# Performance work log

Measured on AMD Instinct MI355X. Metric: run time of the kernel, lower is better.

## Reference

```python
import jax, jax.numpy as jnp
import numpy as np

VOCAB, EMB, HID, LAT = 32000, 512, 1024, 512
B, T = 32, 128


def setup_inputs() -> dict:
    key = jax.random.key(0)
    ks = jax.random.split(key, 10)
    s = 0.02
    return {
        "latent_vector": jax.random.normal(ks[0], (B, LAT), jnp.float32),
        "target_tokens": jax.random.randint(ks[1], (B, T), 0, VOCAB),
        "emb": jax.random.normal(ks[2], (VOCAB, EMB), jnp.float32) * s,
        "W_lh": jax.random.normal(ks[3], (HID, LAT), jnp.float32) * s,
        "b_lh": jnp.zeros((HID,), jnp.float32),
        "W_ih": jax.random.normal(ks[4], (4 * HID, EMB), jnp.float32) * s,
        "b_ih": jnp.zeros((4 * HID,), jnp.float32),
        "W_hh": jax.random.normal(ks[5], (4 * HID, HID), jnp.float32) * s,
        "b_hh": jnp.zeros((4 * HID,), jnp.float32),
        "W_out": jax.random.normal(ks[6], (VOCAB, HID), jnp.float32) * s,
        "b_out": jnp.zeros((VOCAB,), jnp.float32),
    }


def reference(latent_vector, target_tokens, emb, W_lh, b_lh, W_ih, b_ih, W_hh, b_hh, W_out, b_out):
    # teacher_forcing_ratio = 1.0 (deterministic): input at step t is target_tokens[:, t-1]
    h = latent_vector @ W_lh.T + b_lh            # [B, HID]
    c = jnp.zeros_like(h)
    xs = emb[target_tokens[:, :-1]]              # [B, T-1, EMB]
    xs = jnp.swapaxes(xs, 0, 1)                  # [T-1, B, EMB]

    def step(carry, x):
        h, c = carry
        gates = x @ W_ih.T + b_ih + h @ W_hh.T + b_hh   # [B, 4*HID]
        i, f, g, o = jnp.split(gates, 4, axis=-1)       # PyTorch LSTM gate order
        c = jax.nn.sigmoid(f) * c + jax.nn.sigmoid(i) * jnp.tanh(g)
        h = jax.nn.sigmoid(o) * jnp.tanh(c)
        logits = h @ W_out.T + b_out                    # [B, VOCAB]
        return (h, c), logits

    _, logits = jax.lax.scan(step, (h, c), xs)          # [T-1, B, VOCAB]
    return jnp.swapaxes(logits, 0, 1)                   # [B, T-1, VOCAB]
```

## Files before the change

kernel.cpp:

```cpp
#include <hip/hip_runtime.h>
#include <cstdint>

typedef __bf16 bf16x8 __attribute__((ext_vector_type(8)));
typedef __bf16 bf16x4 __attribute__((ext_vector_type(4)));
typedef float  f32x4  __attribute__((ext_vector_type(4)));

#define VOCAB 32000
#define EMB   512
#define HID   1024
#define LAT   512
#define BATCH 32
#define TSTEP 127
#define MROWS 4064
#define MPAD  4096
#define G4    4096
#define NBLK  128
#define FSTRIDE 64

__device__ __forceinline__ float sigf(float x){ return 1.0f / (1.0f + __expf(-x)); }
__device__ __forceinline__ float tanhfast(float x){
    float ax = fabsf(x);
    float e  = __expf(-2.0f * ax);
    float t  = (1.0f - e) / (1.0f + e);
    return copysignf(t, x);
}

__device__ __forceinline__ void gll16(void* lds, const void* gsrc){
    __builtin_amdgcn_global_load_lds(
        (const __attribute__((address_space(1))) unsigned int*)gsrc,
        (__attribute__((address_space(3))) unsigned int*)lds,
        16, 0, 0);
}

__global__ __launch_bounds__(256) void cvt_kernel(
    const float* __restrict__ in, __bf16* __restrict__ out, int n4)
{
    int i = blockIdx.x * 256 + threadIdx.x;
    if (i < n4){
        float4 v = ((const float4*)in)[i];
        bf16x4 o = { (__bf16)v.x, (__bf16)v.y, (__bf16)v.z, (__bf16)v.w };
        ((bf16x4*)out)[i] = o;
    }
}

__global__ __launch_bounds__(256) void init_kernel(
    const float* __restrict__ latent,
    const float* __restrict__ Wlh,
    const float* __restrict__ blh,
    __bf16* __restrict__ h0,
    __bf16* __restrict__ Hall,
    unsigned* __restrict__ flags)
{
    if (blockIdx.x == 0 && threadIdx.x < NBLK)
        flags[threadIdx.x * FSTRIDE] = 0u;

    int id = blockIdx.x * 256 + threadIdx.x;
    int b = id >> 10, j = id & 1023;
    float s = blh[j];
    const float4* lr = (const float4*)(latent + (size_t)b * LAT);
    const float4* wr = (const float4*)(Wlh + (size_t)j * LAT);
    for (int k = 0; k < LAT / 4; ++k){
        float4 a = lr[k], w = wr[k];
        s += a.x * w.x + a.y * w.y + a.z * w.z + a.w * w.w;
    }
    h0[id] = (__bf16)s;
    Hall[(size_t)MROWS * HID + id] = (__bf16)0.0f;
}

__global__ __launch_bounds__(256) void gemm_xg(
    const float* __restrict__ emb,
    const float* __restrict__ Wih,
    const int*   __restrict__ tok,
    float*       __restrict__ xg,
    const float* __restrict__ bih,
    const float* __restrict__ bhh)
{
    __shared__ __bf16 As[2][128 * 32];
    __shared__ __bf16 Bs[2][128 * 32];

    const int tid  = threadIdx.x;
    const int wid  = tid >> 6, lane = tid & 63;
    const int tile_n = blockIdx.x, tile_m = blockIdx.y;
    const int wr = wid >> 1, wc = wid & 1;

    f32x4 acc[4][4] = {};

    auto stage = [&](int kt, int buf){
        #pragma unroll
        for (int j = 0; j < 2; ++j){
            const int slot = tid + j * 256;
            const int row  = slot >> 2;
            const int kb   = kt * 32 + (slot & 3) * 8;
            {
                const int brow = tile_n * 128 + row;
                const float4* p = (const float4*)(Wih + (size_t)brow * EMB + kb);
                float4 u = p[0], v = p[1];
                bf16x8 w = { (__bf16)u.x, (__bf16)u.y, (__bf16)u.z, (__bf16)u.w,
                             (__bf16)v.x, (__bf16)v.y, (__bf16)v.z, (__bf16)v.w };
                *(bf16x8*)&Bs[buf][row * 32 + (slot & 3) * 8] = w;
            }
            {
                int r = tile_m * 128 + row;
                int rc = (r < MROWS) ? r : (MROWS - 1);
                int token = tok[(rc & 31) * 128 + (rc >> 5)];
                const float4* p = (const float4*)(emb + (size_t)token * EMB + kb);
                float4 u = p[0], v = p[1];
                bf16x8 w = { (__bf16)u.x, (__bf16)u.y, (__bf16)u.z, (__bf16)u.w,
                             (__bf16)v.x, (__bf16)v.y, (__bf16)v.z, (__bf16)v.w };
                *(bf16x8*)&As[buf][row * 32 + (slot & 3) * 8] = w;
            }
        }
    };

    const int KT = EMB / 32;
    stage(0, 0);
    for (int kt = 0; kt < KT; ++kt){
        const int buf = kt & 1;
        __syncthreads();
        if (kt + 1 < KT) stage(kt + 1, buf ^ 1);
        const __bf16* Abuf = As[buf];
        const __bf16* Bbuf = Bs[buf];
        const int ar = lane & 15, ko = (lane >> 4) * 8;
        bf16x8 av[4], bv[4];
        #pragma unroll
        for (int m = 0; m < 4; ++m)
            av[m] = *(const bf16x8*)&Abuf[(wr * 64 + m * 16 + ar) * 32 + ko];
        #pragma unroll
        for (int n = 0; n < 4; ++n)
            bv[n] = *(const bf16x8*)&Bbuf[(wc * 64 + n * 16 + ar) * 32 + ko];
        #pragma unroll
        for (int m = 0; m < 4; ++m)
            #pragma unroll
            for (int n = 0; n < 4; ++n)
                acc[m][n] = __builtin_amdgcn_mfma_f32_16x16x32_bf16(av[m], bv[n], acc[m][n], 0, 0, 0);
    }

    const int r0 = tile_m * 128 + wr * 64 + ((lane >> 4) << 2);
    const int c0 = tile_n * 128 + wc * 64 + (lane & 15);
    #pragma unroll
    for (int m = 0; m < 4; ++m){
        #pragma unroll
        for (int n = 0; n < 4; ++n){
            const int col = c0 + n * 16;
            float badd = bih[col] + bhh[col];
            #pragma unroll
            for (int q = 0; q < 4; ++q){
                int row = r0 + m * 16 + q;
                xg[(size_t)row * G4 + col] = acc[m][n][q] + badd;
            }
        }
    }
}

template<int BF16B>
__global__ __launch_bounds__(256) void gemm_logits(
    const __bf16* __restrict__ A,
    const float*  __restrict__ Bf,
    const __bf16* __restrict__ Bb,
    float*        __restrict__ C,
    const float*  __restrict__ bias)
{
    __shared__ __bf16 As[2][128 * 32];
    __shared__ __bf16 Bs[2][128 * 32];

    const int tid  = threadIdx.x;
    const int wid  = tid >> 6, lane = tid & 63;
    const int tile_n = blockIdx.x, tile_m = blockIdx.y;
    const int wr = wid >> 1, wc = wid & 1;

    f32x4 acc[4][4] = {};

    auto stage = [&](int kt, int buf){
        const int kb = kt * 32 + (lane & 3) * 8;
        #pragma unroll
        for (int c2 = 0; c2 < 2; ++c2){
            int rA = tile_m * 128 + c2 * 64 + wid * 16 + (lane >> 2);
            gll16(&As[buf][c2 * 2048 + wid * 512], A + (size_t)rA * HID + kb);
            if constexpr (BF16B){
                int rB = tile_n * 128 + c2 * 64 + wid * 16 + (lane >> 2);
                gll16(&Bs[buf][c2 * 2048 + wid * 512], Bb + (size_t)rB * HID + kb);
            }
        }
        if constexpr (!BF16B){
            #pragma unroll
            for (int j = 0; j < 2; ++j){
                const int slot = tid + j * 256;
                const int row  = slot >> 2;
                const int kb2  = kt * 32 + (slot & 3) * 8;
                const int brow = tile_n * 128 + row;
                const float4* p = (const float4*)(Bf + (size_t)brow * HID + kb2);
                float4 u = p[0], v = p[1];
                bf16x8 w = { (__bf16)u.x, (__bf16)u.y, (__bf16)u.z, (__bf16)u.w,
                             (__bf16)v.x, (__bf16)v.y, (__bf16)v.z, (__bf16)v.w };
                *(bf16x8*)&Bs[buf][row * 32 + (slot & 3) * 8] = w;
            }
        }
    };

    const int KT = HID / 32;
    stage(0, 0);
    for (int kt = 0; kt < KT; ++kt){
        const int buf = kt & 1;
        __syncthreads();
        if (kt + 1 < KT) stage(kt + 1, buf ^ 1);
        const __bf16* Abuf = As[buf];
        const __bf16* Bbuf = Bs[buf];
        const int ar = lane & 15, ko = (lane >> 4) * 8;
        bf16x8 av[4], bv[4];
        #pragma unroll
        for (int m = 0; m < 4; ++m)
            av[m] = *(const bf16x8*)&Abuf[(wr * 64 + m * 16 + ar) * 32 + ko];
        #pragma unroll
        for (int n = 0; n < 4; ++n)
            bv[n] = *(const bf16x8*)&Bbuf[(wc * 64 + n * 16 + ar) * 32 + ko];
        #pragma unroll
        for (int m = 0; m < 4; ++m)
            #pragma unroll
            for (int n = 0; n < 4; ++n)
                acc[m][n] = __builtin_amdgcn_mfma_f32_16x16x32_bf16(av[m], bv[n], acc[m][n], 0, 0, 0);
    }

    const int r0 = tile_m * 128 + wr * 64 + ((lane >> 4) << 2);
    const int c0 = tile_n * 128 + wc * 64 + (lane & 15);
    #pragma unroll
    for (int m = 0; m < 4; ++m){
        #pragma unroll
        for (int n = 0; n < 4; ++n){
            const int col = c0 + n * 16;
            float badd = bias[col];
            #pragma unroll
            for (int q = 0; q < 4; ++q){
                int row = r0 + m * 16 + q;
                if (row < MROWS){
                    int t = row >> 5, b = row & 31;
                    __builtin_nontemporal_store(acc[m][n][q] + badd,
                        &C[((size_t)b * TSTEP + t) * VOCAB + col]);
                }
            }
        }
    }
}

__global__ __launch_bounds__(256) void lstm_coop(
    const float*  __restrict__ xg,
    __bf16*       __restrict__ Hall,
    __bf16*       __restrict__ hbuf,
    const __bf16* __restrict__ Whhb,
    unsigned*     __restrict__ flags)
{
    __shared__ float lds_g[4 * 4 * 4 * 64];
    const int tid = threadIdx.x, wid = tid >> 6, lane = tid & 63;
    const int jb = blockIdx.x * 8;

    bf16x8 bfrag[2][8];
    {
        const int gl = lane & 15, ko = (lane >> 4) * 8;
        #pragma unroll
        for (int nt = 0; nt < 2; ++nt){
            int gg = nt * 16 + gl;
            const __bf16* base =
                Whhb + (size_t)((gg >> 3) * HID + jb + (gg & 7)) * HID + wid * 256 + ko;
            #pragma unroll
            for (int ks = 0; ks < 8; ++ks)
                bfrag[nt][ks] = *(const bf16x8*)(base + ks * 32);
        }
    }

    const int b2 = tid >> 2, up0 = (tid & 3) * 2;
    const int mt2 = b2 >> 4, r2 = b2 & 15, reg2 = r2 & 3, lb2 = (r2 >> 2) << 4;
    float cst[2] = {0.0f, 0.0f};

    const float* xq = xg + (size_t)b2 * G4 + jb + up0;
    float2 xv[4];
    if (tid < 128){
        #pragma unroll
        for (int g = 0; g < 4; ++g) xv[g] = *(const float2*)(xq + g * HID);
    }

    const size_t e0 = (size_t)(lane & 15) * HID + wid * 256 + (lane >> 4) * 8;

    for (int t = 0; t < TSTEP; ++t){
        unsigned long long* hq = (unsigned long long*)(hbuf + (size_t)(t & 1) * (BATCH * HID));
        union { unsigned long long q[2]; bf16x8 v; } xa[16];
        #pragma unroll
        for (int ks = 0; ks < 8; ++ks){
            size_t q0 = (e0 + (size_t)ks * 32) >> 2;
            size_t q1 = q0 + ((size_t)16 * HID >> 2);
            xa[ks].q[0]     = __hip_atomic_load(hq + q0,     __ATOMIC_RELAXED, __HIP_MEMORY_SCOPE_AGENT);
            xa[ks].q[1]     = __hip_atomic_load(hq + q0 + 1, __ATOMIC_RELAXED, __HIP_MEMORY_SCOPE_AGENT);
            xa[8 + ks].q[0] = __hip_atomic_load(hq + q1,     __ATOMIC_RELAXED, __HIP_MEMORY_SCOPE_AGENT);
            xa[8 + ks].q[1] = __hip_atomic_load(hq + q1 + 1, __ATOMIC_RELAXED, __HIP_MEMORY_SCOPE_AGENT);
        }
        f32x4 a00 = {}, a01 = {}, a10 = {}, a11 = {};
        #pragma unroll
        for (int ks = 0; ks < 8; ++ks){
            a00 = __builtin_amdgcn_mfma_f32_16x16x32_bf16(xa[ks].v,     bfrag[0][ks], a00, 0, 0, 0);
            a01 = __builtin_amdgcn_mfma_f32_16x16x32_bf16(xa[ks].v,     bfrag[1][ks], a01, 0, 0, 0);
            a10 = __builtin_amdgcn_mfma_f32_16x16x32_bf16(xa[8 + ks].v, bfrag[0][ks], a10, 0, 0, 0);
            a11 = __builtin_amdgcn_mfma_f32_16x16x32_bf16(xa[8 + ks].v, bfrag[1][ks], a11, 0, 0, 0);
        }
        #pragma unroll
        for (int q = 0; q < 4; ++q){
            lds_g[((0 * 4 + wid) * 4 + q) * 64 + lane] = a00[q];
            lds_g[((1 * 4 + wid) * 4 + q) * 64 + lane] = a01[q];
            lds_g[((2 * 4 + wid) * 4 + q) * 64 + lane] = a10[q];
            lds_g[((3 * 4 + wid) * 4 + q) * 64 + lane] = a11[q];
        }
        __syncthreads();

        if (tid < 128){
            const float* xn = xq + (size_t)(t + 1) * (BATCH * G4);
            float2 xnew[4];
            #pragma unroll
            for (int g = 0; g < 4; ++g) xnew[g] = *(const float2*)(xn + g * HID);

            float h2[2];
            #pragma unroll
            for (int du = 0; du < 2; ++du){
                int u2 = up0 + du;
                float gate[4];
                #pragma unroll
                for (int ty = 0; ty < 4; ++ty){
                    int gg = ty * 8 + u2;
                    int mtnt = mt2 * 2 + (gg >> 4);
                    int li = lb2 | (gg & 15);
                    float s = 0.0f;
                    #pragma unroll
                    for (int w = 0; w < 4; ++w)
                        s += lds_g[((mtnt * 4 + w) * 4 + reg2) * 64 + li];
                    gate[ty] = s;
                }
                float gi = gate[0] + ((du == 0) ? xv[0].x : xv[0].y);
                float gf = gate[1] + ((du == 0) ? xv[1].x : xv[1].y);
                float gc = gate[2] + ((du == 0) ? xv[2].x : xv[2].y);
                float go = gate[3] + ((du == 0) ? xv[3].x : xv[3].y);
                float c = sigf(gf) * cst[du] + sigf(gi) * tanhfast(gc);
                cst[du] = c;
                h2[du] = sigf(go) * tanhfast(c);
            }
            #pragma unroll
            for (int g = 0; g < 4; ++g) xv[g] = xnew[g];

            union { __bf16 h[2]; unsigned u; } pk;
            pk.h[0] = (__bf16)h2[0]; pk.h[1] = (__bf16)h2[1];
            unsigned* hw = (unsigned*)(hbuf + (size_t)((t + 1) & 1) * (BATCH * HID)
                                       + (size_t)b2 * HID + jb + up0);
            __hip_atomic_store(hw, pk.u, __ATOMIC_RELAXED, __HIP_MEMORY_SCOPE_AGENT);
            *(unsigned*)(Hall + ((size_t)t * BATCH + b2) * HID + jb + up0) = pk.u;
        }

        if (t + 1 == TSTEP) break;

        __syncthreads();
        if (wid == 0){
            if (lane == 0){
                __hip_atomic_store(&flags[blockIdx.x * FSTRIDE], (unsigned)(t + 1),
                                   __ATOMIC_RELAXED, __HIP_MEMORY_SCOPE_AGENT);
            }
            const unsigned tgt = (unsigned)(t + 1);
            for (;;){
                unsigned f0 = __hip_atomic_load(&flags[lane * FSTRIDE],
                                  __ATOMIC_RELAXED, __HIP_MEMORY_SCOPE_AGENT);
                unsigned f1 = __hip_atomic_load(&flags[(lane + 64) * FSTRIDE],
                                  __ATOMIC_RELAXED, __HIP_MEMORY_SCOPE_AGENT);
                if (f0 >= tgt && f1 >= tgt) break;
                __builtin_amdgcn_s_sleep(1);
            }
        }
        __syncthreads();
    }
}

extern "C" void kernel_launch(void* const* d_in, const int* in_sizes, int n_in,
                              void* d_out, int out_size, void* d_ws, size_t ws_size,
                              hipStream_t stream)
{
    const float* latent = (const float*)d_in[0];
    const int*   tokens = (const int*)d_in[1];
    const float* emb    = (const float*)d_in[2];
    const float* Wlh    = (const float*)d_in[3];
    const float* blh    = (const float*)d_in[4];
    const float* Wih    = (const float*)d_in[5];
    const float* bih    = (const float*)d_in[6];
    const float* Whh    = (const float*)d_in[7];
    const float* bhh    = (const float*)d_in[8];
    const float* Wout   = (const float*)d_in[9];
    const float* bout   = (const float*)d_in[10];
    float* out = (float*)d_out;

    const size_t xg_b   = (size_t)MPAD * G4 * 4;
    const size_t hall_b = (size_t)MPAD * HID * 2;
    const size_t whh_b  = (size_t)G4 * HID * 2;
    const size_t wout_b = (size_t)VOCAB * HID * 2;
    const size_t hb_b   = (size_t)2 * BATCH * HID * 2;
    const size_t cnt_b  = (size_t)NBLK * FSTRIDE * 4;

    char* p = (char*)d_ws;
    const bool wsA = ws_size >= xg_b + hall_b + whh_b + wout_b + hb_b + cnt_b;
    const bool wsB = ws_size >= hall_b + whh_b + wout_b + hb_b + cnt_b;

    float* xg;
    if (wsA){ xg = (float*)p; p += xg_b; }
    else    { xg = (float*)d_out; }
    __bf16* Hall = (__bf16*)p; p += hall_b;
    __bf16* Whhb = (__bf16*)p; p += whh_b;
    __bf16* Woutb = nullptr;
    if (wsA || wsB){ Woutb = (__bf16*)p; p += wout_b; }
    __bf16* hbuf = (__bf16*)p; p += hb_b;
    unsigned* flags = (unsigned*)p; p += cnt_b;

    cvt_kernel<<<dim3(G4 * HID / 4 / 256), dim3(256), 0, stream>>>(
        Whh, Whhb, G4 * HID / 4);

    init_kernel<<<dim3(128), dim3(256), 0, stream>>>(latent, Wlh, blh, hbuf, Hall, flags);

    gemm_xg<<<dim3(G4 / 128, MPAD / 128), dim3(256), 0, stream>>>(
        emb, Wih, tokens, xg, bih, bhh);

    if (Woutb)
        cvt_kernel<<<dim3(VOCAB * HID / 4 / 256), dim3(256), 0, stream>>>(
            Wout, Woutb, VOCAB * HID / 4);

    {
        const float*  xgc   = xg;
        __bf16*       hallp = Hall;
        __bf16*       hbp   = hbuf;
        const __bf16* whhp  = Whhb;
        unsigned*     flagp = flags;
        void* args[] = { (void*)&xgc, (void*)&hallp, (void*)&hbp, (void*)&whhp, (void*)&flagp };
        hipLaunchCooperativeKernel((void*)lstm_coop, dim3(NBLK), dim3(256), args, 0, stream);
    }

    if (Woutb)
        gemm_logits<1><<<dim3(VOCAB / 128, MPAD / 128), dim3(256), 0, stream>>>(
            Hall, (const float*)nullptr, Woutb, out, bout);
    else
        gemm_logits<0><<<dim3(VOCAB / 128, MPAD / 128), dim3(256), 0, stream>>>(
            Hall, Wout, (const __bf16*)nullptr, out, bout);
}
```

Baseline: 1.313 ms.

## Overlap W_out bf16 conversion with LSTM and swizzle logits GEMM tile order

```diff
diff --git a/kernel.cpp b/kernel.cpp
--- a/kernel.cpp
+++ b/kernel.cpp
@@ -152,6 +152,8 @@
     }
 }
 
+#define NTM 32
+#define NTN 250
 template<int BF16B>
 __global__ __launch_bounds__(256) void gemm_logits(
     const __bf16* __restrict__ A,
@@ -165,7 +167,13 @@
 
     const int tid  = threadIdx.x;
     const int wid  = tid >> 6, lane = tid & 63;
-    const int tile_n = blockIdx.x, tile_m = blockIdx.y;
+
+    const int bid = blockIdx.x;
+    const int s   = (bid & 7) * (NTM * NTN / 8) + (bid >> 3);
+    const int g   = s / (8 * NTN), rem = s % (8 * NTN);
+    const int tile_m = g * 8 + (rem & 7);
+    const int tile_n = rem >> 3;
+
     const int wr = wid >> 1, wc = wid & 1;
 
     f32x4 acc[4][4] = {};
@@ -246,8 +254,23 @@
     __bf16*       __restrict__ Hall,
     __bf16*       __restrict__ hbuf,
     const __bf16* __restrict__ Whhb,
-    unsigned*     __restrict__ flags)
-{
+    unsigned*     __restrict__ flags,
+    const float*  __restrict__ Woutf,
+    __bf16*       __restrict__ Woutb)
+{
+    if (blockIdx.x >= NBLK){
+        if (Woutb){
+            const int n4 = VOCAB * HID / 4;
+            int i = (blockIdx.x - NBLK) * 256 + threadIdx.x;
+            for (; i < n4; i += NBLK * 256){
+                float4 v = ((const float4*)Woutf)[i];
+                bf16x4 o = { (__bf16)v.x, (__bf16)v.y, (__bf16)v.z, (__bf16)v.w };
+                ((bf16x4*)Woutb)[i] = o;
+            }
+        }
+        return;
+    }
+
     __shared__ float lds_g[4 * 4 * 4 * 64];
     const int tid = threadIdx.x, wid = tid >> 6, lane = tid & 63;
     const int jb = blockIdx.x * 8;
@@ -417,24 +440,23 @@
     gemm_xg<<<dim3(G4 / 128, MPAD / 128), dim3(256), 0, stream>>>(
         emb, Wih, tokens, xg, bih, bhh);
 
-    if (Woutb)
-        cvt_kernel<<<dim3(VOCAB * HID / 4 / 256), dim3(256), 0, stream>>>(
-            Wout, Woutb, VOCAB * HID / 4);
-
     {
         const float*  xgc   = xg;
         __bf16*       hallp = Hall;
         __bf16*       hbp   = hbuf;
         const __bf16* whhp  = Whhb;
         unsigned*     flagp = flags;
-        void* args[] = { (void*)&xgc, (void*)&hallp, (void*)&hbp, (void*)&whhp, (void*)&flagp };
-        hipLaunchCooperativeKernel((void*)lstm_coop, dim3(NBLK), dim3(256), args, 0, stream);
+        const float*  wof   = Wout;
+        __bf16*       wob   = Woutb;
+        void* args[] = { (void*)&xgc, (void*)&hallp, (void*)&hbp, (void*)&whhp,
+                         (void*)&flagp, (void*)&wof, (void*)&wob };
+        hipLaunchCooperativeKernel((void*)lstm_coop, dim3(2 * NBLK), dim3(256), args, 0, stream);
     }
 
     if (Woutb)
-        gemm_logits<1><<<dim3(VOCAB / 128, MPAD / 128), dim3(256), 0, stream>>>(
+        gemm_logits<1><<<dim3(NTM * NTN), dim3(256), 0, stream>>>(
             Hall, (const float*)nullptr, Woutb, out, bout);
     else
-        gemm_logits<0><<<dim3(VOCAB / 128, MPAD / 128), dim3(256), 0, stream>>>(
+        gemm_logits<0><<<dim3(NTM * NTN), dim3(256), 0, stream>>>(
             Hall, Wout, (const __bf16*)nullptr, out, bout);
 }
```

Result: faster. 1.219 ms (-7.1%).
